# Performance work log

Measured on AMD Instinct MI355X. Metric: run time of the kernel, lower is better.

The kernel has to match this reference:

```python
import jax, jax.numpy as jnp
import numpy as np

B, C, H, W, HEADS = 8, 256, 64, 64, 4
EPS = 1e-5  # torch InstanceNorm2d default eps


def conv1x1(x, w):
    # w: [out_c, in_c]; x: [b, in_c, h, w]
    return jnp.einsum('oc,bchw->bohw', w, x)


def maxpool2(x):
    b, c, h, w = x.shape
    return x.reshape(b, c, h // 2, 2, w // 2, 2).max(axis=(3, 5))


def inorm_affine(x, g, b):
    # InstanceNorm2d(affine=True): normalize per (batch, channel) over H,W
    m = jnp.mean(x, axis=(2, 3), keepdims=True)
    v = jnp.mean((x - m) ** 2, axis=(2, 3), keepdims=True)
    return (x - m) * jax.lax.rsqrt(v + EPS) * g[None, :, None, None] + b[None, :, None, None]


def setup_inputs() -> dict:
    key = jax.random.key(0)
    ks = jax.random.split(key, 12)
    s = 1.0 / np.sqrt(C)  # fan-in style scaling for 1x1 conv weights
    return {
        'x': jax.random.normal(ks[0], (B, C, H, W), jnp.float32),
        'theta_w': jax.random.normal(ks[1], (C, C), jnp.float32) * s,
        'phi_w': jax.random.normal(ks[2], (C, C), jnp.float32) * s,
        'g_w': jax.random.normal(ks[3], (C // 2, C), jnp.float32) * s,
        'o_w': jax.random.normal(ks[4], (C, C // 2), jnp.float32) * np.sqrt(2.0 / C),
        'nt_w': 1.0 + 0.1 * jax.random.normal(ks[5], (C,), jnp.float32),
        'nt_b': 0.1 * jax.random.normal(ks[6], (C,), jnp.float32),
        'np_w': 1.0 + 0.1 * jax.random.normal(ks[7], (C,), jnp.float32),
        'np_b': 0.1 * jax.random.normal(ks[8], (C,), jnp.float32),
        'ng_w': 1.0 + 0.1 * jax.random.normal(ks[9], (C // 2,), jnp.float32),
        'ng_b': 0.1 * jax.random.normal(ks[10], (C // 2,), jnp.float32),
        'gamma': jnp.float32(0.5),
    }


def reference(x, theta_w, phi_w, g_w, o_w, nt_w, nt_b, np_w, np_b, ng_w, ng_b, gamma):
    b, c, h, w = x.shape
    n = h * w            # query length
    m = n // 4           # key/value length after 2x2 maxpool
    theta = inorm_affine(conv1x1(x, theta_w), nt_w, nt_b)
    phi = inorm_affine(maxpool2(conv1x1(x, phi_w)), np_w, np_b)
    g = inorm_affine(maxpool2(conv1x1(x, g_w)), ng_w, ng_b)
    # custom head layout: channel dim split as (C//heads, heads), head dim INNER
    theta_ = theta.reshape(b, c // HEADS, HEADS, n)
    phi_ = phi.reshape(b, c // HEADS, HEADS, m)
    g_ = g.reshape(b, (c // 2) // HEADS, HEADS, m)
    beta = jax.nn.softmax(jnp.einsum('bchi,bchj->bhij', theta_, phi_), axis=-1)
    o = jnp.einsum('bchj,bhij->bchi', g_, beta).reshape(b, c // 2, h, w)
    o = conv1x1(o, o_w)
    return gamma * o + x
```

## Files before the change

kernel.cpp:

```cpp
#include <hip/hip_runtime.h>
#include <hip/hip_bf16.h>
#include <math.h>

typedef float f32x4 __attribute__((ext_vector_type(4)));
typedef float f32x16 __attribute__((ext_vector_type(16)));
typedef __bf16 b16x8 __attribute__((ext_vector_type(8)));
typedef __bf16 b16x4 __attribute__((ext_vector_type(4)));
typedef unsigned int u32x2 __attribute__((ext_vector_type(2)));
typedef unsigned int u32x4 __attribute__((ext_vector_type(4)));

#define L2E 1.44269504088896340736f

__global__ void prep_weights(const float* tw, const float* pw, const float* gw,
                             const float* ow, __bf16* Wp, __bf16* OWp) {
    int idx = blockIdx.x * 256 + threadIdx.x;
    if (idx < 640 * 256) {
        int m = idx >> 8, k = idx & 255;
        float v;
        if (m < 256)      { int o = ((m & 63) << 2) + (m >> 6);            v = tw[o * 256 + k]; }
        else if (m < 512) { int mm = m - 256; int o = ((mm & 63) << 2) + (mm >> 6); v = pw[o * 256 + k]; }
        else              { int mm = m - 512; int o = ((mm & 31) << 2) + (mm >> 5); v = gw[o * 256 + k]; }
        Wp[idx] = (__bf16)v;
    } else {
        int j = idx - 640 * 256;
        if (j < 256 * 128) {
            int m = j >> 7, c = j & 127;
            int o = ((c & 31) << 2) + (c >> 5);
            OWp[j] = (__bf16)ow[m * 128 + o];
        }
    }
}

__global__ __launch_bounds__(256) void conv_gemm(const __bf16* __restrict__ Wp,
                                                 const float* __restrict__ x,
                                                 __bf16* theta_t, __bf16* phi_t, __bf16* g_t,
                                                 float* tp1, float* tp2) {
    int b = blockIdx.z, mt = blockIdx.y, nt = blockIdx.x;
    __shared__ __bf16 Al[128 * 40];
    __shared__ __bf16 Bl[128 * 40];
    int tid = threadIdx.x, l = tid & 63, w = tid >> 6;
    int wm = w >> 1, wn = w & 1, lr = l & 15, lg = l >> 4;
    f32x4 acc[4][4];
#pragma unroll
    for (int i = 0; i < 4; i++)
#pragma unroll
        for (int j = 0; j < 4; j++)
#pragma unroll
            for (int r = 0; r < 4; r++) acc[i][j][r] = 0.f;
    const __bf16* Ag = Wp + (size_t)mt * 128 * 256;
    const float* Bx = x + (size_t)b * 1048576 + nt * 128;
    int srow = tid >> 2, scol = (tid & 3) * 8;
    int bn = tid & 127, bk0 = (tid >> 7) * 8;
    b16x8 aR[2];
    float xr[2][8];
#pragma unroll
    for (int hh = 0; hh < 2; hh++)
        aR[hh] = *(const b16x8*)&Ag[(size_t)(srow + hh * 64) * 256 + scol];
#pragma unroll
    for (int u = 0; u < 2; u++)
#pragma unroll
        for (int e = 0; e < 8; e++)
            xr[u][e] = Bx[(size_t)(bk0 + u * 16 + e) * 4096 + bn];
    for (int k0 = 0; k0 < 256; k0 += 32) {
        if (k0) __syncthreads();
#pragma unroll
        for (int hh = 0; hh < 2; hh++)
            *(b16x8*)&Al[(srow + hh * 64) * 40 + scol] = aR[hh];
#pragma unroll
        for (int u = 0; u < 2; u++) {
            b16x8 v;
#pragma unroll
            for (int e = 0; e < 8; e++) v[e] = (__bf16)xr[u][e];
            *(b16x8*)&Bl[bn * 40 + bk0 + u * 16] = v;
        }
        __syncthreads();
        if (k0 < 224) {
#pragma unroll
            for (int hh = 0; hh < 2; hh++)
                aR[hh] = *(const b16x8*)&Ag[(size_t)(srow + hh * 64) * 256 + k0 + 32 + scol];
#pragma unroll
            for (int u = 0; u < 2; u++)
#pragma unroll
                for (int e = 0; e < 8; e++)
                    xr[u][e] = Bx[(size_t)(k0 + 32 + bk0 + u * 16 + e) * 4096 + bn];
        }
        int ko = lg * 8;
        b16x8 af[4], bfr[4];
#pragma unroll
        for (int i = 0; i < 4; i++) af[i]  = *(b16x8*)&Al[(wm * 64 + i * 16 + lr) * 40 + ko];
#pragma unroll
        for (int i = 0; i < 4; i++) bfr[i] = *(b16x8*)&Bl[(wn * 64 + i * 16 + lr) * 40 + ko];
#pragma unroll
        for (int i = 0; i < 4; i++)
#pragma unroll
            for (int j = 0; j < 4; j++)
                acc[i][j] = __builtin_amdgcn_mfma_f32_16x16x32_bf16(af[i], bfr[j], acc[i][j], 0, 0, 0);
    }
    if (mt < 2) {
#pragma unroll
        for (int i = 0; i < 4; i++) {
            float s1v[4], s2v[4];
#pragma unroll
            for (int r = 0; r < 4; r++) {
                float a0 = acc[i][0][r], a1 = acc[i][1][r], a2 = acc[i][2][r], a3 = acc[i][3][r];
                s1v[r] = (a0 + a1) + (a2 + a3);
                s2v[r] = (a0 * a0 + a1 * a1) + (a2 * a2 + a3 * a3);
            }
#pragma unroll
            for (int msk = 1; msk < 16; msk <<= 1)
#pragma unroll
                for (int r = 0; r < 4; r++) {
                    s1v[r] += __shfl_xor(s1v[r], msk, 64);
                    s2v[r] += __shfl_xor(s2v[r], msk, 64);
                }
            if (lr == 0) {
                int row = (b * 32 + nt) * 2 + wn;
#pragma unroll
                for (int r = 0; r < 4; r++) {
                    int ch = mt * 128 + wm * 64 + i * 16 + lg * 4 + r;
                    tp1[row * 256 + ch] = s1v[r];
                    tp2[row * 256 + ch] = s2v[r];
                }
            }
        }
    }
    int rbase = lg * 4;
#pragma unroll
    for (int i = 0; i < 4; i++) {
        int m = mt * 128 + wm * 64 + i * 16 + rbase;
#pragma unroll
        for (int j = 0; j < 4; j++) {
            int p = nt * 128 + wn * 64 + j * 16 + lr;
            b16x4 v;
#pragma unroll
            for (int r = 0; r < 4; r++) v[r] = (__bf16)acc[i][j][r];
            if (m < 256)      *(b16x4*)&theta_t[((size_t)b * 4096 + p) * 256 + m] = v;
            else if (m < 512) *(b16x4*)&phi_t[((size_t)b * 4096 + p) * 256 + (m - 256)] = v;
            else              *(b16x4*)&g_t[((size_t)b * 4096 + p) * 128 + (m - 512)] = v;
        }
    }
}

__global__ __launch_bounds__(256) void pool_phi(const __bf16* __restrict__ src, __bf16* dst,
                                                float* p1, float* p2) {
    __shared__ float S1[8][256], S2[8][256];
    int b = blockIdx.y, qc = blockIdx.x;
    int tid = threadIdx.x, cg = tid & 31, qg = tid >> 5;
    float a1[8], a2[8];
#pragma unroll
    for (int e = 0; e < 8; e++) { a1[e] = 0.f; a2[e] = 0.f; }
#pragma unroll
    for (int qq = 0; qq < 4; qq++) {
        int q = qc * 32 + qg * 4 + qq, qy = q >> 5, qx = q & 31;
        size_t base = ((size_t)(b * 4096) + qy * 128 + qx * 2) * 256 + cg * 8;
        b16x8 v0 = *(const b16x8*)&src[base];
        b16x8 v1 = *(const b16x8*)&src[base + 256];
        b16x8 v2 = *(const b16x8*)&src[base + 16384];
        b16x8 v3 = *(const b16x8*)&src[base + 16640];
        b16x8 mv;
#pragma unroll
        for (int e = 0; e < 8; e++) {
            float m = fmaxf(fmaxf((float)v0[e], (float)v1[e]), fmaxf((float)v2[e], (float)v3[e]));
            mv[e] = (__bf16)m; a1[e] += m; a2[e] += m * m;
        }
        *(b16x8*)&dst[((size_t)b * 1024 + q) * 256 + cg * 8] = mv;
    }
#pragma unroll
    for (int e = 0; e < 8; e++) { S1[qg][cg * 8 + e] = a1[e]; S2[qg][cg * 8 + e] = a2[e]; }
    __syncthreads();
    float s1 = 0.f, s2 = 0.f;
#pragma unroll
    for (int i = 0; i < 8; i++) { s1 += S1[i][tid]; s2 += S2[i][tid]; }
    p1[(b * 32 + qc) * 256 + tid] = s1;
    p2[(b * 32 + qc) * 256 + tid] = s2;
}

__global__ __launch_bounds__(256) void pool_gT(const __bf16* __restrict__ src, __bf16* gT,
                                               float* p1, float* p2) {
    __shared__ __bf16 Pt[64][136];
    __shared__ float S1[16][128], S2[16][128];
    int b = blockIdx.y, qc = blockIdx.x;
    int tid = threadIdx.x, cg = tid & 15, qg = tid >> 4;
    float a1[8], a2[8];
#pragma unroll
    for (int e = 0; e < 8; e++) { a1[e] = 0.f; a2[e] = 0.f; }
#pragma unroll
    for (int qq = 0; qq < 4; qq++) {
        int ql = qg * 4 + qq, q = qc * 64 + ql;
        int qy = q >> 5, qx = q & 31;
        size_t base = ((size_t)(b * 4096) + qy * 128 + qx * 2) * 128 + cg * 8;
        b16x8 v0 = *(const b16x8*)&src[base];
        b16x8 v1 = *(const b16x8*)&src[base + 128];
        b16x8 v2 = *(const b16x8*)&src[base + 8192];
        b16x8 v3 = *(const b16x8*)&src[base + 8320];
        b16x8 mv;
#pragma unroll
        for (int e = 0; e < 8; e++) {
            float m = fmaxf(fmaxf((float)v0[e], (float)v1[e]), fmaxf((float)v2[e], (float)v3[e]));
            mv[e] = (__bf16)m; a1[e] += m; a2[e] += m * m;
        }
        *(b16x8*)&Pt[ql][cg * 8] = mv;
    }
#pragma unroll
    for (int e = 0; e < 8; e++) { S1[qg][cg * 8 + e] = a1[e]; S2[qg][cg * 8 + e] = a2[e]; }
    __syncthreads();
    if (tid < 128) {
        float s1 = 0.f, s2 = 0.f;
#pragma unroll
        for (int i = 0; i < 16; i++) { s1 += S1[i][tid]; s2 += S2[i][tid]; }
        p1[(b * 16 + qc) * 128 + tid] = s1;
        p2[(b * 16 + qc) * 128 + tid] = s2;
    }
    int c = tid & 127, qh = tid >> 7;
    int hh = c >> 5, ch = c & 31;
#pragma unroll
    for (int sg = 0; sg < 4; sg++) {
        int seg = qh * 4 + sg;
        b16x8 v;
#pragma unroll
        for (int e = 0; e < 8; e++) v[e] = Pt[seg * 8 + e][c];
        *(b16x8*)&gT[((((size_t)(b * 4 + hh) * 16 + qc) * 8 + seg) * 32 + ch) * 8] = v;
    }
}

__global__ void finalize_stats(const float* tp1, const float* tp2, const float* pp1,
                               const float* pp2, const float* gp1, const float* gp2,
                               const float* ntw, const float* ntb, const float* npw,
                               const float* npb, const float* ngw, const float* ngb,
                               float* sct, float* bit, float* scp, float* bip,
                               float* scg, float* big) {
    int idx = blockIdx.x * 256 + threadIdx.x;
    if (idx >= 8 * 640) return;
    int b = idx / 640, c = idx % 640;
    if (c < 256) {
        float s1 = 0.f, s2 = 0.f;
        for (int i = 0; i < 64; i++) { s1 += tp1[(b * 64 + i) * 256 + c]; s2 += tp2[(b * 64 + i) * 256 + c]; }
        float n = 4096.f;
        float m = s1 / n, v = s2 / n - m * m;
        float r = rsqrtf(v + 1e-5f);
        int o = ((c & 63) << 2) + (c >> 6);
        float wv = ntw[o], bv = ntb[o];
        sct[b * 256 + c] = r * wv * L2E;
        bit[b * 256 + c] = (bv - m * r * wv) * L2E;
    } else if (c < 512) {
        int cc = c - 256;
        float s1 = 0.f, s2 = 0.f;
        for (int i = 0; i < 32; i++) { s1 += pp1[(b * 32 + i) * 256 + cc]; s2 += pp2[(b * 32 + i) * 256 + cc]; }
        float n = 1024.f;
        float m = s1 / n, v = s2 / n - m * m;
        float r = rsqrtf(v + 1e-5f);
        int o = ((cc & 63) << 2) + (cc >> 6);
        float wv = npw[o], bv = npb[o];
        scp[b * 256 + cc] = r * wv; bip[b * 256 + cc] = bv - m * r * wv;
    } else {
        int cc = c - 512;
        float s1 = 0.f, s2 = 0.f;
        for (int i = 0; i < 16; i++) { s1 += gp1[(b * 16 + i) * 128 + cc]; s2 += gp2[(b * 16 + i) * 128 + cc]; }
        float n = 1024.f;
        float m = s1 / n, v = s2 / n - m * m;
        float r = rsqrtf(v + 1e-5f);
        int o = ((cc & 31) << 2) + (cc >> 5);
        float wv = ngw[o], bv = ngb[o];
        scg[b * 128 + cc] = r * wv; big[b * 128 + cc] = bv - m * r * wv;
    }
}

__global__ void normalize_phi(const __bf16* __restrict__ php, __bf16* __restrict__ phk,
                              const float* __restrict__ scp, const float* __restrict__ bip) {
    int blk = blockIdx.x, t = threadIdx.x;
    int b = blk >> 6, h = (blk >> 4) & 3, cc = blk & 15;
#pragma unroll
    for (int uu = 0; uu < 2; uu++) {
        int u = uu * 256 + t;
        int slot = u >> 6, key = u & 63;
        int q = cc * 64 + key;
        int cfull = h * 64 + (slot >> 1) * 16 + (slot & 1) * 8;
        b16x8 v = *(const b16x8*)&php[((size_t)b * 1024 + q) * 256 + cfull];
        b16x8 nv;
#pragma unroll
        for (int e = 0; e < 8; e++)
            nv[e] = (__bf16)((float)v[e] * scp[b * 256 + cfull + e] + bip[b * 256 + cfull + e]);
        *(b16x8*)&phk[((((size_t)(b * 4 + h) * 16 + cc) * 8 + slot) * 64 + key) * 8] = nv;
    }
}

__global__ __launch_bounds__(256) void attn(const __bf16* __restrict__ theta_t,
                                            const __bf16* __restrict__ phk,
                                            const __bf16* __restrict__ gTz,
                                            const float* __restrict__ sct,
                                            const float* __restrict__ bit,
                                            const float* __restrict__ scg,
                                            const float* __restrict__ big,
                                            __bf16* __restrict__ o_mid) {
    int bid = blockIdx.x;
    int idx = bid >> 3;
    int bh = (bid & 7) * 4 + (idx >> 5), qt = idx & 31;
    int b = bh >> 2, h = bh & 3;
    int tid = threadIdx.x, w = tid >> 6, lane = tid & 63;
    int l31 = lane & 31, hi = lane >> 5;
    int q = qt * 128 + w * 32 + l31;

    b16x8 qf[4];
    {
        const __bf16* qp = theta_t + ((size_t)b * 4096 + q) * 256 + h * 64;
#pragma unroll
        for (int st = 0; st < 4; st++) {
            int cb = st * 16 + hi * 8;
            b16x8 raw = *(const b16x8*)&qp[cb];
            b16x8 nv;
#pragma unroll
            for (int e = 0; e < 8; e++) {
                int cix = b * 256 + h * 64 + cb + e;
                nv[e] = (__bf16)((float)raw[e] * sct[cix] + bit[cix]);
            }
            qf[st] = nv;
        }
    }

    const __bf16* Kg = phk + (size_t)bh * 65536 + hi * 512 + l31 * 8;
    const __bf16* Vg = gTz + (size_t)bh * 32768 + hi * 256 + l31 * 8;

    f32x16 oacc;
    float l_run = 0.f;
#pragma unroll
    for (int r = 0; r < 16; r++) oacc[r] = 0.f;
    f32x16 zc;
#pragma unroll
    for (int r = 0; r < 16; r++) zc[r] = 0.f;

    b16x8 ak[2][4], av[4], avn[4];

#define LOADK(dst, c) { _Pragma("unroll") for (int kf = 0; kf < 2; kf++) \
    _Pragma("unroll") for (int st = 0; st < 4; st++) \
        dst[kf][st] = *(const b16x8*)&Kg[(size_t)(c) * 4096 + st * 1024 + kf * 256]; }
#define LOADV(dst, c) { _Pragma("unroll") for (int js = 0; js < 4; js++) \
    dst[js] = *(const b16x8*)&Vg[(size_t)(c) * 2048 + js * 512]; }

    LOADK(ak, 0) LOADV(av, 0)
#pragma unroll 1
    for (int c = 0; c < 16; ++c) {
        f32x16 s[2];
#pragma unroll
        for (int kf = 0; kf < 2; kf++) {
            s[kf] = __builtin_amdgcn_mfma_f32_32x32x16_bf16(ak[kf][0], qf[0], zc, 0, 0, 0);
#pragma unroll
            for (int st = 1; st < 4; st++)
                s[kf] = __builtin_amdgcn_mfma_f32_32x32x16_bf16(ak[kf][st], qf[st], s[kf], 0, 0, 0);
        }
        if (c < 15) { LOADK(ak, c + 1) }
        float s0 = 0.f, s1 = 0.f, s2p = 0.f, s3 = 0.f;
#pragma unroll
        for (int kf = 0; kf < 2; kf++)
#pragma unroll
            for (int r = 0; r < 16; r += 4) {
                float p0 = __builtin_amdgcn_exp2f(s[kf][r]);
                float p1 = __builtin_amdgcn_exp2f(s[kf][r + 1]);
                float p2 = __builtin_amdgcn_exp2f(s[kf][r + 2]);
                float p3 = __builtin_amdgcn_exp2f(s[kf][r + 3]);
                s[kf][r] = p0; s[kf][r + 1] = p1; s[kf][r + 2] = p2; s[kf][r + 3] = p3;
                s0 += p0; s1 += p1; s2p += p2; s3 += p3;
            }
        l_run += (s0 + s1) + (s2p + s3);
        if (c < 15) { LOADV(avn, c + 1) }
#pragma unroll
        for (int kf = 0; kf < 2; kf++)
#pragma unroll
            for (int hh2 = 0; hh2 < 2; hh2++) {
                b16x4 A4, B4;
#pragma unroll
                for (int e = 0; e < 4; e++) {
                    A4[e] = (__bf16)s[kf][hh2 * 8 + e];
                    B4[e] = (__bf16)s[kf][hh2 * 8 + 4 + e];
                }
                u32x2 a2 = __builtin_bit_cast(u32x2, A4);
                u32x2 b2 = __builtin_bit_cast(u32x2, B4);
                u32x2 q0 = __builtin_amdgcn_permlane32_swap(a2[0], b2[0], false, false);
                u32x2 q1 = __builtin_amdgcn_permlane32_swap(a2[1], b2[1], false, false);
                u32x4 pd = {q0[0], q1[0], q0[1], q1[1]};
                b16x8 pf = __builtin_bit_cast(b16x8, pd);
                oacc = __builtin_amdgcn_mfma_f32_32x32x16_bf16(av[kf * 2 + hh2], pf, oacc, 0, 0, 0);
            }
        if (c < 15) {
#pragma unroll
            for (int js = 0; js < 4; js++) av[js] = avn[js];
        }
    }
#undef LOADK
#undef LOADV

    {
        float lr = l_run + __shfl_xor(l_run, 32, 64);
        float rl = 1.0f / lr;
#pragma unroll
        for (int rr = 0; rr < 4; rr++) {
            b16x4 v;
#pragma unroll
            for (int e = 0; e < 4; e++) {
                int ci = b * 128 + h * 32 + rr * 8 + hi * 4 + e;
                v[e] = (__bf16)(oacc[rr * 4 + e] * rl * scg[ci] + big[ci]);
            }
            *(b16x4*)&o_mid[((size_t)b * 4096 + q) * 128 + h * 32 + rr * 8 + hi * 4] = v;
        }
    }
}

__global__ __launch_bounds__(256) void out_gemm(const __bf16* __restrict__ OWp,
                                                const __bf16* __restrict__ o_mid,
                                                const float* __restrict__ x,
                                                const float* gamma, float* out) {
    int b = blockIdx.z, mt = blockIdx.y, nt = blockIdx.x;
    __shared__ __bf16 Al[128 * 40];
    __shared__ __bf16 Bl[128 * 40];
    int tid = threadIdx.x, l = tid & 63, w = tid >> 6;
    int wm = w >> 1, wn = w & 1, lr = l & 15, lg = l >> 4;
    f32x4 acc[4][4];
#pragma unroll
    for (int i = 0; i < 4; i++)
#pragma unroll
        for (int j = 0; j < 4; j++)
#pragma unroll
            for (int r = 0; r < 4; r++) acc[i][j][r] = 0.f;
    const __bf16* Ag = OWp + (size_t)mt * 128 * 128;
    const __bf16* Bg = o_mid + ((size_t)b * 4096 + nt * 128) * 128;
    int srow = tid >> 2, scol = (tid & 3) * 8;
    b16x8 aR[2], bR[2];
#pragma unroll
    for (int hh = 0; hh < 2; hh++) {
        int r = srow + hh * 64;
        aR[hh] = *(const b16x8*)&Ag[(size_t)r * 128 + scol];
        bR[hh] = *(const b16x8*)&Bg[(size_t)r * 128 + scol];
    }
    for (int k0 = 0; k0 < 128; k0 += 32) {
        if (k0) __syncthreads();
#pragma unroll
        for (int hh = 0; hh < 2; hh++) {
            int r = srow + hh * 64;
            *(b16x8*)&Al[r * 40 + scol] = aR[hh];
            *(b16x8*)&Bl[r * 40 + scol] = bR[hh];
        }
        __syncthreads();
        if (k0 < 96) {
#pragma unroll
            for (int hh = 0; hh < 2; hh++) {
                int r = srow + hh * 64;
                aR[hh] = *(const b16x8*)&Ag[(size_t)r * 128 + k0 + 32 + scol];
                bR[hh] = *(const b16x8*)&Bg[(size_t)r * 128 + k0 + 32 + scol];
            }
        }
        int ko = lg * 8;
        b16x8 af[4], bfr[4];
#pragma unroll
        for (int i = 0; i < 4; i++) af[i]  = *(b16x8*)&Al[(wm * 64 + i * 16 + lr) * 40 + ko];
#pragma unroll
        for (int i = 0; i < 4; i++) bfr[i] = *(b16x8*)&Bl[(wn * 64 + i * 16 + lr) * 40 + ko];
#pragma unroll
        for (int i = 0; i < 4; i++)
#pragma unroll
            for (int j = 0; j < 4; j++)
                acc[i][j] = __builtin_amdgcn_mfma_f32_16x16x32_bf16(af[i], bfr[j], acc[i][j], 0, 0, 0);
    }
    float gm = gamma[0];
    int rbase = lg * 4;
#pragma unroll
    for (int i = 0; i < 4; i++) {
        int m = mt * 128 + wm * 64 + i * 16 + rbase;
#pragma unroll
        for (int j = 0; j < 4; j++) {
            int p = nt * 128 + wn * 64 + j * 16 + lr;
#pragma unroll
            for (int r = 0; r < 4; r++) {
                size_t o = ((size_t)b * 256 + m + r) * 4096 + p;
                __builtin_nontemporal_store(gm * acc[i][j][r] + x[o], &out[o]);
            }
        }
    }
}

extern "C" void kernel_launch(void* const* d_in, const int* in_sizes, int n_in,
                              void* d_out, int out_size, void* d_ws, size_t ws_size,
                              hipStream_t stream) {
    const float* x   = (const float*)d_in[0];
    const float* tw  = (const float*)d_in[1];
    const float* pw  = (const float*)d_in[2];
    const float* gw  = (const float*)d_in[3];
    const float* ow  = (const float*)d_in[4];
    const float* ntw = (const float*)d_in[5];
    const float* ntb = (const float*)d_in[6];
    const float* npw = (const float*)d_in[7];
    const float* npb = (const float*)d_in[8];
    const float* ngw = (const float*)d_in[9];
    const float* ngb = (const float*)d_in[10];
    const float* gamma = (const float*)d_in[11];
    float* out = (float*)d_out;
    char* ws = (char*)d_ws;

    __bf16* Wp  = (__bf16*)(ws + 0);
    __bf16* OWp = (__bf16*)(ws + 327680);
    __bf16* th  = (__bf16*)(ws + 17170432);
    __bf16* phr = (__bf16*)(ws + 33947648);
    __bf16* ghr = (__bf16*)(ws + 50724864);
    __bf16* php = (__bf16*)(ws + 59113472);
    __bf16* gT  = (__bf16*)(ws + 63307776);
    float* sb   = (float*)(ws + 65445888);

    float* tp1 = (float*)(ws + 393216);
    float* tp2 = (float*)(ws + 917504);
    float* pp1 = (float*)(ws + 1441792);
    float* pp2 = (float*)(ws + 1703936);
    float* gp1 = (float*)(ws + 1966080);
    float* gp2 = (float*)(ws + 2031616);
    __bf16* phk = phr;
    __bf16* om  = (__bf16*)(ws + 2097152);

    float *sct = sb, *bit = sb + 2048, *scp = sb + 4096, *bip = sb + 6144,
          *scg = sb + 8192, *big = sb + 9216;

    prep_weights<<<768, 256, 0, stream>>>(tw, pw, gw, ow, Wp, OWp);
    conv_gemm<<<dim3(32, 5, 8), 256, 0, stream>>>(Wp, x, th, phr, ghr, tp1, tp2);
    pool_phi<<<dim3(32, 8), 256, 0, stream>>>(phr, php, pp1, pp2);
    pool_gT<<<dim3(16, 8), 256, 0, stream>>>(ghr, gT, gp1, gp2);
    finalize_stats<<<20, 256, 0, stream>>>(tp1, tp2, pp1, pp2, gp1, gp2,
                                           ntw, ntb, npw, npb, ngw, ngb,
                                           sct, bit, scp, bip, scg, big);
    normalize_phi<<<512, 256, 0, stream>>>(php, phk, scp, bip);
    attn<<<1024, 256, 0, stream>>>(th, phk, gT, sct, bit, scg, big, om);
    out_gemm<<<dim3(32, 2, 8), 256, 0, stream>>>(OWp, om, x, gamma, out);
}
```

Before: 124.4 us.

## Process two query tiles per wave in attention to reuse K/V loads

Each wave now handles 64 queries (two 32-row tiles) instead of 32, so every K and V fragment loaded from global memory feeds twice as many MFMAs. The grid is halved to 512 blocks. The key loop is restructured into a ping-pong double buffer (A/B register sets) rather than the single prefetch buffer with a copy. This doubles accumulator and query register usage, with launch bounds set to 2 blocks per CU, and halves the number of blocks available to fill the GPU.

```diff
diff --git a/kernel.cpp b/kernel.cpp
--- a/kernel.cpp
+++ b/kernel.cpp
@@ -284,24 +284,26 @@
     }
 }
 
-__global__ __launch_bounds__(256) void attn(const __bf16* __restrict__ theta_t,
-                                            const __bf16* __restrict__ phk,
-                                            const __bf16* __restrict__ gTz,
-                                            const float* __restrict__ sct,
-                                            const float* __restrict__ bit,
-                                            const float* __restrict__ scg,
-                                            const float* __restrict__ big,
-                                            __bf16* __restrict__ o_mid) {
+__global__ __launch_bounds__(256, 2) void attn(const __bf16* __restrict__ theta_t,
+                                               const __bf16* __restrict__ phk,
+                                               const __bf16* __restrict__ gTz,
+                                               const float* __restrict__ sct,
+                                               const float* __restrict__ bit,
+                                               const float* __restrict__ scg,
+                                               const float* __restrict__ big,
+                                               __bf16* __restrict__ o_mid) {
     int bid = blockIdx.x;
     int idx = bid >> 3;
-    int bh = (bid & 7) * 4 + (idx >> 5), qt = idx & 31;
+    int bh = (bid & 7) * 4 + (idx >> 4), qt = idx & 15;
     int b = bh >> 2, h = bh & 3;
     int tid = threadIdx.x, w = tid >> 6, lane = tid & 63;
     int l31 = lane & 31, hi = lane >> 5;
-    int q = qt * 128 + w * 32 + l31;
-
-    b16x8 qf[4];
-    {
+    int qb = qt * 256 + w * 64;
+
+    b16x8 qf[2][4];
+#pragma unroll
+    for (int m = 0; m < 2; m++) {
+        int q = qb + m * 32 + l31;
         const __bf16* qp = theta_t + ((size_t)b * 4096 + q) * 256 + h * 64;
 #pragma unroll
         for (int st = 0; st < 4; st++) {
@@ -313,91 +315,79 @@
                 int cix = b * 256 + h * 64 + cb + e;
                 nv[e] = (__bf16)((float)raw[e] * sct[cix] + bit[cix]);
             }
-            qf[st] = nv;
-        }
-    }
-
-    const __bf16* Kg = phk + (size_t)bh * 65536 + hi * 512 + l31 * 8;
-    const __bf16* Vg = gTz + (size_t)bh * 32768 + hi * 256 + l31 * 8;
-
-    f32x16 oacc;
-    float l_run = 0.f;
-#pragma unroll
-    for (int r = 0; r < 16; r++) oacc[r] = 0.f;
+            qf[m][st] = nv;
+        }
+    }
+
+    const __bf16* Kg = phk + (size_t)bh * 65536 + (size_t)hi * 512 + (size_t)l31 * 8;
+    const __bf16* Vg = gTz + (size_t)bh * 32768 + (size_t)hi * 256 + (size_t)l31 * 8;
+
+    f32x16 oacc[2];
+    float l_run[2] = {0.f, 0.f};
+#pragma unroll
+    for (int m = 0; m < 2; m++)
+#pragma unroll
+        for (int r = 0; r < 16; r++) oacc[m][r] = 0.f;
     f32x16 zc;
 #pragma unroll
     for (int r = 0; r < 16; r++) zc[r] = 0.f;
 
-    b16x8 ak[2][4], av[4], avn[4];
+    b16x8 akA[2][4], avA[4], akB[2][4], avB[4];
 
 #define LOADK(dst, c) { _Pragma("unroll") for (int kf = 0; kf < 2; kf++) \
     _Pragma("unroll") for (int st = 0; st < 4; st++) \
         dst[kf][st] = *(const b16x8*)&Kg[(size_t)(c) * 4096 + st * 1024 + kf * 256]; }
 #define LOADV(dst, c) { _Pragma("unroll") for (int js = 0; js < 4; js++) \
     dst[js] = *(const b16x8*)&Vg[(size_t)(c) * 2048 + js * 512]; }
-
-    LOADK(ak, 0) LOADV(av, 0)
+#define COMPUTE(ak, av) { \
+    _Pragma("unroll") for (int m = 0; m < 2; m++) { \
+        _Pragma("unroll") for (int kf = 0; kf < 2; kf++) { \
+            f32x16 s = __builtin_amdgcn_mfma_f32_32x32x16_bf16(ak[kf][0], qf[m][0], zc, 0, 0, 0); \
+            _Pragma("unroll") for (int st = 1; st < 4; st++) \
+                s = __builtin_amdgcn_mfma_f32_32x32x16_bf16(ak[kf][st], qf[m][st], s, 0, 0, 0); \
+            float sum = 0.f; \
+            _Pragma("unroll") for (int r = 0; r < 16; r++) { \
+                float p = __builtin_amdgcn_exp2f(s[r]); s[r] = p; sum += p; } \
+            l_run[m] += sum; \
+            _Pragma("unroll") for (int hh2 = 0; hh2 < 2; hh2++) { \
+                b16x4 A4, B4; \
+                _Pragma("unroll") for (int e = 0; e < 4; e++) { \
+                    A4[e] = (__bf16)s[hh2 * 8 + e]; B4[e] = (__bf16)s[hh2 * 8 + 4 + e]; } \
+                u32x2 a2 = __builtin_bit_cast(u32x2, A4); \
+                u32x2 b2 = __builtin_bit_cast(u32x2, B4); \
+                u32x2 q0 = __builtin_amdgcn_permlane32_swap(a2[0], b2[0], false, false); \
+                u32x2 q1 = __builtin_amdgcn_permlane32_swap(a2[1], b2[1], false, false); \
+                u32x4 pd = {q0[0], q1[0], q0[1], q1[1]}; \
+                b16x8 pf = __builtin_bit_cast(b16x8, pd); \
+                oacc[m] = __builtin_amdgcn_mfma_f32_32x32x16_bf16(av[kf * 2 + hh2], pf, oacc[m], 0, 0, 0); \
+            } \
+        } \
+    } }
+
+    LOADK(akA, 0) LOADV(avA, 0)
 #pragma unroll 1
-    for (int c = 0; c < 16; ++c) {
-        f32x16 s[2];
-#pragma unroll
-        for (int kf = 0; kf < 2; kf++) {
-            s[kf] = __builtin_amdgcn_mfma_f32_32x32x16_bf16(ak[kf][0], qf[0], zc, 0, 0, 0);
-#pragma unroll
-            for (int st = 1; st < 4; st++)
-                s[kf] = __builtin_amdgcn_mfma_f32_32x32x16_bf16(ak[kf][st], qf[st], s[kf], 0, 0, 0);
-        }
-        if (c < 15) { LOADK(ak, c + 1) }
-        float s0 = 0.f, s1 = 0.f, s2p = 0.f, s3 = 0.f;
-#pragma unroll
-        for (int kf = 0; kf < 2; kf++)
-#pragma unroll
-            for (int r = 0; r < 16; r += 4) {
-                float p0 = __builtin_amdgcn_exp2f(s[kf][r]);
-                float p1 = __builtin_amdgcn_exp2f(s[kf][r + 1]);
-                float p2 = __builtin_amdgcn_exp2f(s[kf][r + 2]);
-                float p3 = __builtin_amdgcn_exp2f(s[kf][r + 3]);
-                s[kf][r] = p0; s[kf][r + 1] = p1; s[kf][r + 2] = p2; s[kf][r + 3] = p3;
-                s0 += p0; s1 += p1; s2p += p2; s3 += p3;
-            }
-        l_run += (s0 + s1) + (s2p + s3);
-        if (c < 15) { LOADV(avn, c + 1) }
-#pragma unroll
-        for (int kf = 0; kf < 2; kf++)
-#pragma unroll
-            for (int hh2 = 0; hh2 < 2; hh2++) {
-                b16x4 A4, B4;
-#pragma unroll
-                for (int e = 0; e < 4; e++) {
-                    A4[e] = (__bf16)s[kf][hh2 * 8 + e];
-                    B4[e] = (__bf16)s[kf][hh2 * 8 + 4 + e];
-                }
-                u32x2 a2 = __builtin_bit_cast(u32x2, A4);
-                u32x2 b2 = __builtin_bit_cast(u32x2, B4);
-                u32x2 q0 = __builtin_amdgcn_permlane32_swap(a2[0], b2[0], false, false);
-                u32x2 q1 = __builtin_amdgcn_permlane32_swap(a2[1], b2[1], false, false);
-                u32x4 pd = {q0[0], q1[0], q0[1], q1[1]};
-                b16x8 pf = __builtin_bit_cast(b16x8, pd);
-                oacc = __builtin_amdgcn_mfma_f32_32x32x16_bf16(av[kf * 2 + hh2], pf, oacc, 0, 0, 0);
-            }
-        if (c < 15) {
-#pragma unroll
-            for (int js = 0; js < 4; js++) av[js] = avn[js];
-        }
+    for (int c = 0; c < 16; c += 2) {
+        LOADK(akB, c + 1) LOADV(avB, c + 1)
+        COMPUTE(akA, avA)
+        if (c + 2 < 16) { LOADK(akA, c + 2) LOADV(avA, c + 2) }
+        COMPUTE(akB, avB)
     }
 #undef LOADK
 #undef LOADV
-
-    {
-        float lr = l_run + __shfl_xor(l_run, 32, 64);
+#undef COMPUTE
+
+#pragma unroll
+    for (int m = 0; m < 2; m++) {
+        float lr = l_run[m] + __shfl_xor(l_run[m], 32, 64);
         float rl = 1.0f / lr;
+        int q = qb + m * 32 + l31;
 #pragma unroll
         for (int rr = 0; rr < 4; rr++) {
             b16x4 v;
 #pragma unroll
             for (int e = 0; e < 4; e++) {
                 int ci = b * 128 + h * 32 + rr * 8 + hi * 4 + e;
-                v[e] = (__bf16)(oacc[rr * 4 + e] * rl * scg[ci] + big[ci]);
+                v[e] = (__bf16)(oacc[m][rr * 4 + e] * rl * scg[ci] + big[ci]);
             }
             *(b16x4*)&o_mid[((size_t)b * 4096 + q) * 128 + h * 32 + rr * 8 + hi * 4] = v;
         }
@@ -523,6 +513,6 @@
                                            ntw, ntb, npw, npb, ngw, ngb,
                                            sct, bit, scp, bip, scg, big);
     normalize_phi<<<512, 256, 0, stream>>>(php, phk, scp, bip);
-    attn<<<1024, 256, 0, stream>>>(th, phk, gT, sct, bit, scg, big, om);
+    attn<<<512, 256, 0, stream>>>(th, phk, gT, sct, bit, scg, big, om);
     out_gemm<<<dim3(32, 2, 8), 256, 0, stream>>>(OWp, om, x, gamma, out);
 }
```

New measurement: 115.7 us. 7.0% less time.
